# Performance work log

Hardware: AMD Instinct MI355X
Metric: run time of the kernel (lower is better)

## Reference

```python
import jax, jax.numpy as jnp
import numpy as np

T, D_IN, D_OUT, R, A = 8192, 4096, 4096, 16, 8  # tokens, in/out features, lora rank, n_adapters/segments


def setup_inputs() -> dict:
    key = jax.random.key(0)
    ks = jax.random.split(key, 8)
    x = jax.random.normal(ks[0], (T, D_IN), jnp.float32)
    base_w = jax.random.normal(ks[1], (D_OUT, D_IN), jnp.float32) * (D_IN ** -0.5)
    base_b = jax.random.normal(ks[2], (D_OUT,), jnp.float32)
    wa = jax.random.normal(ks[3], (A, D_IN, R), jnp.float32) * (D_IN ** -0.5)
    wb = jax.random.normal(ks[4], (A, R, D_OUT), jnp.float32) * (R ** -0.5)
    scaling = jax.random.uniform(ks[5], (A,), jnp.float32, 0.5, 2.0)
    inner = jnp.sort(jax.random.randint(ks[6], (A - 1,), 0, T)).astype(jnp.int32)
    segment = jnp.concatenate([jnp.zeros(1, jnp.int32), inner, jnp.full((1,), T, jnp.int32)])  # [A+1] boundaries
    lora_ids = jax.random.randint(ks[7], (A,), 0, A).astype(jnp.int32)  # adapter id per segment
    return {"x": x, "base_w": base_w, "base_b": base_b, "wa": wa, "wb": wb,
            "scaling": scaling, "segment": segment, "lora_ids": lora_ids}


def reference(x, base_w, base_b, wa, wb, scaling, segment, lora_ids):
    # base dense layer: result = base_layer(x)
    result = x @ base_w.T + base_b  # [T, D_OUT]
    # per-token segment id (segments are contiguous token ranges), then adapter id
    token_pos = jnp.arange(x.shape[0])
    token_seg = jnp.clip(jnp.searchsorted(segment, token_pos, side='right') - 1, 0, segment.shape[0] - 2)
    token_lora = lora_ids[token_seg]  # [T] adapter id per token
    # grouped rank-r GEMM (SGMV-style add_lora): h_t = x_t @ wa[id_t]; lora_t = h_t @ wb[id_t]
    onehot = jax.nn.one_hot(token_lora, wa.shape[0], dtype=x.dtype)  # [T, A]
    h = jnp.einsum('td,adr->tar', x, wa) * onehot[:, :, None]  # [T, A, R], masked to own adapter
    lora = jnp.einsum('tar,aro->to', h, wb)  # [T, D_OUT]
    # per-token scaling = repeat_interleave(scaling[lora_ids], lora_len)
    lora = lora * scaling[token_lora][:, None]
    return result + lora
```

## Files before the change

### kernel.cpp

```cpp
#include <hip/hip_runtime.h>

#define T_TOK 8192
#define DIN   4096
#define DOUTF 4096
#define RANK  16

#define BM 256
#define BN 256
#define BK 128
#define NT (DIN / BK)
#define NPAIR (NT / 2)

typedef __attribute__((ext_vector_type(4))) float f32x4;
typedef __attribute__((ext_vector_type(4))) int   i32x4;
typedef __attribute__((ext_vector_type(8))) short bf16x8;

#define GLB_PTR(p) ((const __attribute__((address_space(1))) void*)(p))
#define LDS_PTR(p) ((__attribute__((address_space(3))) void*)(p))

__device__ __forceinline__ unsigned short f2bf(float f) {
  unsigned u = __float_as_uint(f);
  u = (u + 0x7fffu + ((u >> 16) & 1u)) >> 16;
  return (unsigned short)u;
}

__global__ __launch_bounds__(256) void prep(const float* __restrict__ x,
                                            const float* __restrict__ base_w,
                                            const float* __restrict__ wa,
                                            const float* __restrict__ scaling,
                                            const int* __restrict__ segment,
                                            const int* __restrict__ lora_ids,
                                            signed char* __restrict__ xq,
                                            float* __restrict__ sx,
                                            signed char* __restrict__ wq,
                                            float* __restrict__ sw,
                                            float* __restrict__ hbuf,
                                            unsigned short* __restrict__ hb16,
                                            int* __restrict__ tokid) {
  const int lane = threadIdx.x & 63;
  const int wave = threadIdx.x >> 6;

  if (blockIdx.x >= 512) {
    const int row = (blockIdx.x - 512) * 4 + wave;
    const float* rp = base_w + (size_t)row * DIN;
    f32x4 v[16];
    float amax = 0.f;
#pragma unroll
    for (int it = 0; it < 16; ++it) {
      v[it] = *(const f32x4*)(rp + it * 256 + lane * 4);
#pragma unroll
      for (int e = 0; e < 4; ++e) amax = fmaxf(amax, fabsf(v[it][e]));
    }
#pragma unroll
    for (int o = 1; o < 64; o <<= 1) amax = fmaxf(amax, __shfl_xor(amax, o));
    const float inv = amax > 0.f ? 127.0f / amax : 0.f;
    if (lane == 0) sw[row] = amax * (1.0f / 127.0f);
    signed char* op = wq + (size_t)row * DIN;
#pragma unroll
    for (int it = 0; it < 16; ++it) {
      const int q0 = (int)rintf(v[it][0] * inv);
      const int q1 = (int)rintf(v[it][1] * inv);
      const int q2 = (int)rintf(v[it][2] * inv);
      const int q3 = (int)rintf(v[it][3] * inv);
      *(int*)(op + it * 256 + lane * 4) =
          (q0 & 255) | ((q1 & 255) << 8) | ((q2 & 255) << 16) | ((q3 & 255) << 24);
    }
    return;
  }

  const int t0 = blockIdx.x * 16 + wave * 4;

  int ids[4]; float sc[4];
#pragma unroll
  for (int q = 0; q < 4; ++q) {
    int t = t0 + q;
    int s = 0;
#pragma unroll
    for (int i = 1; i < 8; ++i)
      if (t >= segment[i]) s = i;
    int id = lora_ids[s];
    ids[q] = id;
    sc[q] = scaling[id];
  }

  float acc[4][16];
  float amax[4] = {0.f, 0.f, 0.f, 0.f};
#pragma unroll
  for (int q = 0; q < 4; ++q)
#pragma unroll
    for (int r = 0; r < 16; ++r) acc[q][r] = 0.f;

  const bool same = (ids[0] == ids[1]) && (ids[1] == ids[2]) && (ids[2] == ids[3]);
  const int dbase = lane * 4;

  if (same) {
    const float* wrow = wa + (size_t)ids[0] * DIN * RANK;
#pragma unroll 2
    for (int it = 0; it < 16; ++it) {
      const int d = it * 256 + dbase;
      f32x4 xv[4];
#pragma unroll
      for (int q = 0; q < 4; ++q) {
        xv[q] = *(const f32x4*)(x + (size_t)(t0 + q) * DIN + d);
#pragma unroll
        for (int e = 0; e < 4; ++e) amax[q] = fmaxf(amax[q], fabsf(xv[q][e]));
      }
#pragma unroll
      for (int dd = 0; dd < 4; ++dd) {
        const f32x4* wp = (const f32x4*)(wrow + (size_t)(d + dd) * RANK);
        f32x4 w0 = wp[0], w1 = wp[1], w2 = wp[2], w3 = wp[3];
#pragma unroll
        for (int q = 0; q < 4; ++q) {
          const float xs = xv[q][dd];
#pragma unroll
          for (int r = 0; r < 4; ++r) {
            acc[q][r]      += xs * w0[r];
            acc[q][r + 4]  += xs * w1[r];
            acc[q][r + 8]  += xs * w2[r];
            acc[q][r + 12] += xs * w3[r];
          }
        }
      }
    }
  } else {
#pragma unroll
    for (int q = 0; q < 4; ++q) {
      const float* wrow = wa + (size_t)ids[q] * DIN * RANK;
      for (int it = 0; it < 16; ++it) {
        const int d = it * 256 + dbase;
        f32x4 xv = *(const f32x4*)(x + (size_t)(t0 + q) * DIN + d);
#pragma unroll
        for (int e = 0; e < 4; ++e) amax[q] = fmaxf(amax[q], fabsf(xv[e]));
#pragma unroll
        for (int dd = 0; dd < 4; ++dd) {
          const f32x4* wp = (const f32x4*)(wrow + (size_t)(d + dd) * RANK);
          f32x4 w0 = wp[0], w1 = wp[1], w2 = wp[2], w3 = wp[3];
          const float xs = xv[dd];
#pragma unroll
          for (int r = 0; r < 4; ++r) {
            acc[q][r]      += xs * w0[r];
            acc[q][r + 4]  += xs * w1[r];
            acc[q][r + 8]  += xs * w2[r];
            acc[q][r + 12] += xs * w3[r];
          }
        }
      }
    }
  }

#pragma unroll
  for (int q = 0; q < 4; ++q) {
#pragma unroll
    for (int r = 0; r < 16; ++r) {
      float v = acc[q][r];
      v += __shfl_xor(v, 1);
      v += __shfl_xor(v, 2);
      v += __shfl_xor(v, 4);
      v += __shfl_xor(v, 8);
      v += __shfl_xor(v, 16);
      v += __shfl_xor(v, 32);
      acc[q][r] = v;
    }
    if (lane == 0) {
      int t = t0 + q;
      tokid[t] = ids[q];
#pragma unroll
      for (int r = 0; r < 16; ++r) {
        float v = sc[q] * acc[q][r];
        hbuf[t * RANK + r] = v;
        hb16[t * RANK + r] = f2bf(v);
      }
    }
  }

#pragma unroll
  for (int q = 0; q < 4; ++q) {
    float am = amax[q];
#pragma unroll
    for (int o = 1; o < 64; o <<= 1) am = fmaxf(am, __shfl_xor(am, o));
    const float inv = am > 0.f ? 127.0f / am : 0.f;
    if (lane == 0) sx[t0 + q] = am * (1.0f / 127.0f);
    const float* rp = x + (size_t)(t0 + q) * DIN;
    signed char* op = xq + (size_t)(t0 + q) * DIN;
#pragma unroll 4
    for (int it = 0; it < 16; ++it) {
      f32x4 v = *(const f32x4*)(rp + it * 256 + dbase);
      const int q0 = (int)rintf(v[0] * inv);
      const int q1 = (int)rintf(v[1] * inv);
      const int q2 = (int)rintf(v[2] * inv);
      const int q3 = (int)rintf(v[3] * inv);
      *(int*)(op + it * 256 + dbase) =
          (q0 & 255) | ((q1 & 255) << 8) | ((q2 & 255) << 16) | ((q3 & 255) << 24);
    }
  }
}

__global__ __launch_bounds__(512, 2) void gemm_fused(const signed char* __restrict__ A_,
                                                     const signed char* __restrict__ B_,
                                                     const float* __restrict__ bias,
                                                     const float* __restrict__ hbuf,
                                                     const unsigned short* __restrict__ hb16,
                                                     const int* __restrict__ tokid,
                                                     const float* __restrict__ wbt,
                                                     const float* __restrict__ sxv,
                                                     const float* __restrict__ swv,
                                                     float* __restrict__ out) {
  __shared__ __align__(16) signed char As[2][BM * BK];
  __shared__ __align__(16) signed char Bs[2][BN * BK];
  __shared__ int s_nb;

  const int tid = threadIdx.x;
  const int lane = tid & 63;
  const int wave = tid >> 6;
  const int wr = wave >> 2;
  const int wn = wave & 3;

  const int bsw = (blockIdx.x & 7) * 64 + (blockIdx.x >> 3);
  const int brow = (bsw >> 4) * BM;
  const int bcol = (bsw & 15) * BN;

  i32x4 acc[8][4] = {};

  const int g = lane >> 4;
  const int rsel = lane & 15;
  const int low3 = rsel & 7;

#define STAGE1(dst, bufp, h, tt, src, rb0)                                             \
  {                                                                                    \
    _Pragma("unroll")                                                                  \
    for (int i = 0; i < 2; ++i) {                                                      \
      const int lin2 = i * 512 + tid;                                                  \
      const int rr = lin2 >> 3;                                                        \
      const int klog = ((lin2 & 7) ^ (rr & 7)) * 16;                        \
      const signed char* gp = (src) + (size_t)((rb0) + (h) * 128 + rr) * DIN + (tt) * BK + klog; \
      __builtin_amdgcn_global_load_lds(GLB_PTR(gp), LDS_PTR(&dst[bufp][(h) * 16384 + lin2 * 16]), 16, 0, 0); \
    }                                                                                  \
  }

#define RD_B(p)                                                                        \
  _Pragma("unroll") for (int kk = 0; kk < 2; ++kk)                                     \
  _Pragma("unroll") for (int n = 0; n < 4; ++n)                                        \
    bfr[n][kk] = *(const i32x4*)(&Bs[p][(wn * 64 + n * 16 + rsel) * BK + (((kk) * 4 + g) ^ low3) * 16]);

#define RD_A(AF, p, mo, kk)                                                            \
  _Pragma("unroll") for (int mi = 0; mi < 4; ++mi)                                     \
    AF[mi] = *(const i32x4*)(&As[p][(wr * 128 + ((mo) + mi) * 16 + rsel) * BK + (((kk) * 4 + g) ^ low3) * 16]);

#define MFMA16(mo, kk, AF)                                                             \
  _Pragma("unroll") for (int mi = 0; mi < 4; ++mi)                                     \
  _Pragma("unroll") for (int n = 0; n < 4; ++n)                                        \
    acc[(mo) + mi][n] = __builtin_amdgcn_mfma_i32_16x16x64_i8(AF[mi], bfr[n][kk],      \
                                                              acc[(mo) + mi][n], 0, 0, 0)

#define PH_OPEN()                                                                      \
  asm volatile("" ::: "memory");                                                       \
  __builtin_amdgcn_s_barrier();                                                        \
  asm volatile("s_waitcnt lgkmcnt(0)" ::: "memory");                                   \
  __builtin_amdgcn_sched_barrier(0);                                                   \
  __builtin_amdgcn_s_setprio(1)

#define PH_CLOSE()                                                                     \
  __builtin_amdgcn_s_setprio(0);                                                       \
  asm volatile("" ::: "memory");                                                       \
  __builtin_amdgcn_s_barrier();                                                        \
  asm volatile("" ::: "memory")

#define PH_CLOSE_VM(N)                                                                 \
  __builtin_amdgcn_s_setprio(0);                                                       \
  asm volatile("s_waitcnt vmcnt(" #N ")" ::: "memory");                                \
  __builtin_amdgcn_s_barrier();                                                        \
  asm volatile("" ::: "memory")

  STAGE1(As, 0, 0, 0, A_, brow);
  STAGE1(As, 0, 1, 0, A_, brow);
  STAGE1(Bs, 0, 0, 0, B_, bcol);
  STAGE1(Bs, 0, 1, 0, B_, bcol);
  STAGE1(Bs, 1, 0, 1, B_, bcol);
  STAGE1(Bs, 1, 1, 1, B_, bcol);
  asm volatile("s_waitcnt vmcnt(4)" ::: "memory");
  __builtin_amdgcn_s_barrier();
  asm volatile("" ::: "memory");

  for (int j = 0; j < NPAIR - 1; ++j) {
    const int v = 2 * j + 1;
    i32x4 bfr[4][2], afA[4], afB[4];
    RD_B(0); RD_A(afA, 0, 0, 0);
    STAGE1(As, 1, 0, v, A_, brow);
    PH_OPEN(); MFMA16(0, 0, afA); PH_CLOSE();
    RD_A(afB, 0, 4, 0);
    STAGE1(As, 1, 1, v, A_, brow);
    PH_OPEN(); MFMA16(4, 0, afB); PH_CLOSE();
    RD_A(afA, 0, 0, 1);
    STAGE1(Bs, 0, 0, v + 1, B_, bcol);
    PH_OPEN(); MFMA16(0, 1, afA); PH_CLOSE();
    RD_A(afB, 0, 4, 1);
    STAGE1(Bs, 0, 1, v + 1, B_, bcol);
    PH_OPEN(); MFMA16(4, 1, afB); PH_CLOSE_VM(4);
    RD_B(1); RD_A(afA, 1, 0, 0);
    STAGE1(As, 0, 0, v + 1, A_, brow);
    PH_OPEN(); MFMA16(0, 0, afA); PH_CLOSE();
    RD_A(afB, 1, 4, 0);
    STAGE1(As, 0, 1, v + 1, A_, brow);
    PH_OPEN(); MFMA16(4, 0, afB); PH_CLOSE();
    RD_A(afA, 1, 0, 1);
    STAGE1(Bs, 1, 0, v + 2, B_, bcol);
    PH_OPEN(); MFMA16(0, 1, afA); PH_CLOSE();
    RD_A(afB, 1, 4, 1);
    STAGE1(Bs, 1, 1, v + 2, B_, bcol);
    PH_OPEN(); MFMA16(4, 1, afB); PH_CLOSE_VM(4);
  }

  {
    const int v = NT - 1;
    i32x4 bfr[4][2], afA[4], afB[4];
    RD_B(0); RD_A(afA, 0, 0, 0);
    STAGE1(As, 1, 0, v, A_, brow);
    PH_OPEN(); MFMA16(0, 0, afA); PH_CLOSE();
    RD_A(afB, 0, 4, 0);
    STAGE1(As, 1, 1, v, A_, brow);
    PH_OPEN(); MFMA16(4, 0, afB); PH_CLOSE();
    RD_A(afA, 0, 0, 1);
    PH_OPEN(); MFMA16(0, 1, afA); PH_CLOSE();
    RD_A(afB, 0, 4, 1);
    PH_OPEN(); MFMA16(4, 1, afB); PH_CLOSE_VM(0);
    RD_B(1); RD_A(afA, 1, 0, 0);
    PH_OPEN(); MFMA16(0, 0, afA); PH_CLOSE();
    RD_A(afB, 1, 4, 0);
    PH_OPEN(); MFMA16(4, 0, afB); PH_CLOSE();
    RD_A(afA, 1, 0, 1);
    PH_OPEN(); MFMA16(0, 1, afA); PH_CLOSE();
    RD_A(afB, 1, 4, 1);
    PH_OPEN(); MFMA16(4, 1, afB); PH_CLOSE();
  }

  const int rb = brow + wr * 128;
  const int cb = bcol + wn * 64;
  const int crow = g * 4;
  const int ccol = rsel;

  if (tid == 0) s_nb = 0;
  __syncthreads();
  if (tid >= 1 && tid < BM) {
    if (tokid[brow + tid] != tokid[brow + tid - 1]) atomicAdd(&s_nb, 1);
  }
  __syncthreads();
  const int nb = s_nb;
  const int idLo = tokid[brow];
  const int idHi = tokid[brow + BM - 1];

  float biasn[4], swn[4];
#pragma unroll
  for (int n = 0; n < 4; ++n) {
    biasn[n] = bias[cb + n * 16 + ccol];
    swn[n] = swv[cb + n * 16 + ccol];
  }

  f32x4 facc[8][4];
#pragma unroll
  for (int m = 0; m < 8; ++m) {
    float sxr[4];
#pragma unroll
    for (int jj = 0; jj < 4; ++jj) sxr[jj] = sxv[rb + m * 16 + crow + jj];
#pragma unroll
    for (int n = 0; n < 4; ++n)
#pragma unroll
      for (int jj = 0; jj < 4; ++jj)
        facc[m][n][jj] = (float)acc[m][n][jj] * (sxr[jj] * swn[n]);
  }

  if (nb <= 1) {
    const int myId = (g < 2) ? idLo : idHi;
    const int maskId = (g < 2) ? idLo : ((nb == 0) ? 0x80000000 : idHi);
    const float* wbase = wbt + (size_t)myId * RANK * DOUTF + (size_t)((g & 1) * 8) * DOUTF;
    bf16x8 bext[4];
#pragma unroll
    for (int n = 0; n < 4; ++n) {
      const int col = cb + n * 16 + ccol;
#pragma unroll
      for (int jj = 0; jj < 8; ++jj)
        bext[n][jj] = (short)f2bf(wbase[(size_t)jj * DOUTF + col]);
    }
#pragma unroll
    for (int m = 0; m < 8; ++m) {
      const int row = rb + m * 16 + rsel;
      const int rid = tokid[row];
      bf16x8 av = {};
      if (rid == maskId)
        av = *(const bf16x8*)(hb16 + (size_t)row * RANK + (g & 1) * 8);
#pragma unroll
      for (int n = 0; n < 4; ++n)
        facc[m][n] = __builtin_amdgcn_mfma_f32_16x16x32_bf16(av, bext[n], facc[m][n], 0, 0, 0);
    }
#pragma unroll
    for (int m = 0; m < 8; ++m) {
#pragma unroll
      for (int jj = 0; jj < 4; ++jj) {
        const int row = rb + m * 16 + crow + jj;
        float* orow = out + (size_t)row * DOUTF;
#pragma unroll
        for (int n = 0; n < 4; ++n)
          orow[cb + n * 16 + ccol] = facc[m][n][jj] + biasn[n];
      }
    }
  } else {
#pragma unroll
    for (int m = 0; m < 8; ++m) {
#pragma unroll
      for (int jj = 0; jj < 4; ++jj) {
        const int row = rb + m * 16 + crow + jj;
        const float4* hp = (const float4*)(hbuf + (size_t)row * RANK);
        float4 h0 = hp[0], h1 = hp[1], h2 = hp[2], h3 = hp[3];
        float hv[16] = {h0.x, h0.y, h0.z, h0.w, h1.x, h1.y, h1.z, h1.w,
                        h2.x, h2.y, h2.z, h2.w, h3.x, h3.y, h3.z, h3.w};
        const float* wrow = wbt + (size_t)tokid[row] * RANK * DOUTF;
        float* orow = out + (size_t)row * DOUTF;
#pragma unroll
        for (int n = 0; n < 4; ++n) {
          const int col = cb + n * 16 + ccol;
          float vsum = facc[m][n][jj] + biasn[n];
#pragma unroll
          for (int r = 0; r < 16; ++r) vsum += hv[r] * wrow[(size_t)r * DOUTF + col];
          orow[col] = vsum;
        }
      }
    }
  }
#undef STAGE1
#undef RD_A
#undef RD_B
#undef MFMA16
#undef PH_OPEN
#undef PH_CLOSE
#undef PH_CLOSE_VM
}

extern "C" void kernel_launch(void* const* d_in, const int* in_sizes, int n_in,
                              void* d_out, int out_size, void* d_ws, size_t ws_size,
                              hipStream_t stream) {
  const float* x       = (const float*)d_in[0];
  const float* base_w  = (const float*)d_in[1];
  const float* base_b  = (const float*)d_in[2];
  const float* wa      = (const float*)d_in[3];
  const float* wb      = (const float*)d_in[4];
  const float* scaling = (const float*)d_in[5];
  const int*   segment = (const int*)d_in[6];
  const int*   lora_id = (const int*)d_in[7];
  float* out = (float*)d_out;

  char* ws = (char*)d_ws;
  signed char* xq = (signed char*)ws;
  signed char* wq = (signed char*)(ws + (size_t)T_TOK * DIN);
  float* sx   = (float*)(ws + (size_t)T_TOK * DIN + (size_t)DOUTF * DIN);
  float* sw   = sx + T_TOK;
  float* hbuf = sw + DOUTF;
  int* tokid  = (int*)(hbuf + (size_t)T_TOK * RANK);
  unsigned short* hb16 = (unsigned short*)(tokid + T_TOK);

  prep<<<512 + DOUTF / 4, 256, 0, stream>>>(x, base_w, wa, scaling, segment, lora_id,
                                            xq, sx, wq, sw, hbuf, hb16, tokid);
  gemm_fused<<<(T_TOK / BM) * (DOUTF / BN), 512, 0, stream>>>(xq, wq, base_b, hbuf,
                                                              hb16, tokid, wb, sx, sw,
                                                              out);
}
```

Baseline: 299.0 us.

## Compute LoRA-A projection in prep with bf16 MFMA over 64-token blocks

The prep kernel's token path now handles 64 tokens per block instead of 16. Each block builds the list of adapters present in its tokens, stages each adapter's wa chunk in LDS as bf16, and computes the rank-16 projection with 16x16x32 bf16 MFMA instructions instead of scalar FMAs with cross-lane shuffle reductions. The int8 quantisation of x is rewritten so each thread writes 16 bytes per row. This reduces the ALU and shuffle work in the h computation, but it lowers h precision to bf16 inputs, re-reads x for every adapter present in the block, and adds block-level syncs.

Result: slower. 328.8 us (+10.0%).

```diff
diff --git a/kernel.cpp b/kernel.cpp
--- a/kernel.cpp
+++ b/kernel.cpp
@@ -37,11 +37,12 @@
                                             float* __restrict__ hbuf,
                                             unsigned short* __restrict__ hb16,
                                             int* __restrict__ tokid) {
-  const int lane = threadIdx.x & 63;
-  const int wave = threadIdx.x >> 6;
-
-  if (blockIdx.x >= 512) {
-    const int row = (blockIdx.x - 512) * 4 + wave;
+  const int tid = threadIdx.x;
+  const int lane = tid & 63;
+  const int wave = tid >> 6;
+
+  if (blockIdx.x >= 128) {
+    const int row = (blockIdx.x - 128) * 4 + wave;
     const float* rp = base_w + (size_t)row * DIN;
     f32x4 v[16];
     float amax = 0.f;
@@ -68,130 +69,124 @@
     return;
   }
 
-  const int t0 = blockIdx.x * 16 + wave * 4;
-
-  int ids[4]; float sc[4];
-#pragma unroll
-  for (int q = 0; q < 4; ++q) {
-    int t = t0 + q;
+  __shared__ __align__(16) unsigned short wch[16][520];
+  __shared__ float amax_l[64];
+  __shared__ int ids_l[64];
+  __shared__ int alist[8];
+  __shared__ int s_na;
+
+  const int T0 = blockIdx.x * 64;
+  const int Tw = T0 + wave * 16;
+  const int r15 = lane & 15;
+  const int kg = lane >> 4;
+
+  if (tid < 64) {
+    const int t = T0 + tid;
     int s = 0;
 #pragma unroll
     for (int i = 1; i < 8; ++i)
       if (t >= segment[i]) s = i;
-    int id = lora_ids[s];
-    ids[q] = id;
-    sc[q] = scaling[id];
-  }
-
-  float acc[4][16];
-  float amax[4] = {0.f, 0.f, 0.f, 0.f};
-#pragma unroll
-  for (int q = 0; q < 4; ++q)
-#pragma unroll
-    for (int r = 0; r < 16; ++r) acc[q][r] = 0.f;
-
-  const bool same = (ids[0] == ids[1]) && (ids[1] == ids[2]) && (ids[2] == ids[3]);
-  const int dbase = lane * 4;
-
-  if (same) {
-    const float* wrow = wa + (size_t)ids[0] * DIN * RANK;
-#pragma unroll 2
-    for (int it = 0; it < 16; ++it) {
-      const int d = it * 256 + dbase;
-      f32x4 xv[4];
-#pragma unroll
-      for (int q = 0; q < 4; ++q) {
-        xv[q] = *(const f32x4*)(x + (size_t)(t0 + q) * DIN + d);
-#pragma unroll
-        for (int e = 0; e < 4; ++e) amax[q] = fmaxf(amax[q], fabsf(xv[q][e]));
-      }
-#pragma unroll
-      for (int dd = 0; dd < 4; ++dd) {
-        const f32x4* wp = (const f32x4*)(wrow + (size_t)(d + dd) * RANK);
-        f32x4 w0 = wp[0], w1 = wp[1], w2 = wp[2], w3 = wp[3];
-#pragma unroll
-        for (int q = 0; q < 4; ++q) {
-          const float xs = xv[q][dd];
-#pragma unroll
-          for (int r = 0; r < 4; ++r) {
-            acc[q][r]      += xs * w0[r];
-            acc[q][r + 4]  += xs * w1[r];
-            acc[q][r + 8]  += xs * w2[r];
-            acc[q][r + 12] += xs * w3[r];
-          }
+    ids_l[tid] = lora_ids[s];
+  }
+  __syncthreads();
+  if (tid == 0) {
+    int na = 0;
+    for (int i = 0; i < 64; ++i) {
+      const int id = ids_l[i];
+      bool dup = false;
+      for (int q = 0; q < na; ++q) dup = dup || (alist[q] == id);
+      if (!dup) alist[na++] = id;
+    }
+    s_na = na;
+  }
+  __syncthreads();
+
+  const int myId = ids_l[wave * 16 + r15];
+  const int myTok = Tw + r15;
+  const int na = s_na;
+
+  f32x4 hacc = {0.f, 0.f, 0.f, 0.f};
+  float amax = 0.f;
+
+  for (int ai = 0; ai < na; ++ai) {
+    const int a = alist[ai];
+    const float* wabase = wa + (size_t)a * (DIN * RANK);
+    const unsigned long long mm = __ballot(myId == a);
+    const bool active = (mm != 0ull);
+    for (int c = 0; c < 8; ++c) {
+      __syncthreads();
+      {
+        const float* gp = wabase + (size_t)(c * 512 + 2 * tid) * RANK;
+        f32x4 w[8];
+#pragma unroll
+        for (int i = 0; i < 8; ++i) w[i] = *(const f32x4*)(gp + i * 4);
+#pragma unroll
+        for (int r = 0; r < 16; ++r) {
+          const unsigned lo = f2bf(w[r >> 2][r & 3]);
+          const unsigned hi = f2bf(w[4 + (r >> 2)][r & 3]);
+          *(unsigned*)&wch[r][2 * tid] = lo | (hi << 16);
         }
       }
-    }
-  } else {
-#pragma unroll
-    for (int q = 0; q < 4; ++q) {
-      const float* wrow = wa + (size_t)ids[q] * DIN * RANK;
-      for (int it = 0; it < 16; ++it) {
-        const int d = it * 256 + dbase;
-        f32x4 xv = *(const f32x4*)(x + (size_t)(t0 + q) * DIN + d);
-#pragma unroll
-        for (int e = 0; e < 4; ++e) amax[q] = fmaxf(amax[q], fabsf(xv[e]));
-#pragma unroll
-        for (int dd = 0; dd < 4; ++dd) {
-          const f32x4* wp = (const f32x4*)(wrow + (size_t)(d + dd) * RANK);
-          f32x4 w0 = wp[0], w1 = wp[1], w2 = wp[2], w3 = wp[3];
-          const float xs = xv[dd];
-#pragma unroll
-          for (int r = 0; r < 4; ++r) {
-            acc[q][r]      += xs * w0[r];
-            acc[q][r + 4]  += xs * w1[r];
-            acc[q][r + 8]  += xs * w2[r];
-            acc[q][r + 12] += xs * w3[r];
+      __syncthreads();
+      if (ai == 0 || active) {
+#pragma unroll 4
+        for (int s = 0; s < 16; ++s) {
+          const int kl = s * 32 + kg * 8;
+          const float* xp = x + (size_t)myTok * DIN + c * 512 + kl;
+          f32x4 x0 = *(const f32x4*)xp;
+          f32x4 x1 = *(const f32x4*)(xp + 4);
+          if (ai == 0) {
+#pragma unroll
+            for (int e = 0; e < 4; ++e)
+              amax = fmaxf(amax, fmaxf(fabsf(x0[e]), fabsf(x1[e])));
           }
+          bf16x8 af;
+#pragma unroll
+          for (int e = 0; e < 4; ++e) {
+            af[e] = (short)f2bf(x0[e]);
+            af[4 + e] = (short)f2bf(x1[e]);
+          }
+          if (myId != a) af = (bf16x8){0, 0, 0, 0, 0, 0, 0, 0};
+          const bf16x8 bf = *(const bf16x8*)&wch[r15][kl];
+          hacc = __builtin_amdgcn_mfma_f32_16x16x32_bf16(af, bf, hacc, 0, 0, 0);
         }
       }
     }
   }
 
-#pragma unroll
-  for (int q = 0; q < 4; ++q) {
-#pragma unroll
-    for (int r = 0; r < 16; ++r) {
-      float v = acc[q][r];
-      v += __shfl_xor(v, 1);
-      v += __shfl_xor(v, 2);
-      v += __shfl_xor(v, 4);
-      v += __shfl_xor(v, 8);
-      v += __shfl_xor(v, 16);
-      v += __shfl_xor(v, 32);
-      acc[q][r] = v;
-    }
-    if (lane == 0) {
-      int t = t0 + q;
-      tokid[t] = ids[q];
-#pragma unroll
-      for (int r = 0; r < 16; ++r) {
-        float v = sc[q] * acc[q][r];
-        hbuf[t * RANK + r] = v;
-        hb16[t * RANK + r] = f2bf(v);
-      }
-    }
-  }
-
-#pragma unroll
-  for (int q = 0; q < 4; ++q) {
-    float am = amax[q];
-#pragma unroll
-    for (int o = 1; o < 64; o <<= 1) am = fmaxf(am, __shfl_xor(am, o));
+  amax = fmaxf(amax, __shfl_xor(amax, 16));
+  amax = fmaxf(amax, __shfl_xor(amax, 32));
+  if (lane < 16) amax_l[wave * 16 + lane] = amax;
+
+#pragma unroll
+  for (int e = 0; e < 4; ++e) {
+    const int li = wave * 16 + kg * 4 + e;
+    const int t = T0 + li;
+    const float sc = scaling[ids_l[li]];
+    const float hv = hacc[e] * sc;
+    hbuf[t * RANK + r15] = hv;
+    hb16[t * RANK + r15] = f2bf(hv);
+  }
+
+  __syncthreads();
+  if (tid < 64) {
+    sx[T0 + tid] = amax_l[tid] * (1.0f / 127.0f);
+    tokid[T0 + tid] = ids_l[tid];
+  }
+
+  for (int row = 0; row < 64; ++row) {
+    const float am = amax_l[row];
     const float inv = am > 0.f ? 127.0f / am : 0.f;
-    if (lane == 0) sx[t0 + q] = am * (1.0f / 127.0f);
-    const float* rp = x + (size_t)(t0 + q) * DIN;
-    signed char* op = xq + (size_t)(t0 + q) * DIN;
-#pragma unroll 4
-    for (int it = 0; it < 16; ++it) {
-      f32x4 v = *(const f32x4*)(rp + it * 256 + dbase);
-      const int q0 = (int)rintf(v[0] * inv);
-      const int q1 = (int)rintf(v[1] * inv);
-      const int q2 = (int)rintf(v[2] * inv);
-      const int q3 = (int)rintf(v[3] * inv);
-      *(int*)(op + it * 256 + dbase) =
-          (q0 & 255) | ((q1 & 255) << 8) | ((q2 & 255) << 16) | ((q3 & 255) << 24);
-    }
+    const float* rp = x + (size_t)(T0 + row) * DIN + tid * 16;
+    signed char* op = xq + (size_t)(T0 + row) * DIN + tid * 16;
+    i32x4 pk;
+#pragma unroll
+    for (int i = 0; i < 4; ++i) {
+      f32x4 v = *(const f32x4*)(rp + i * 4);
+      pk[i] = ((int)rintf(v[0] * inv) & 255) | (((int)rintf(v[1] * inv) & 255) << 8) |
+              (((int)rintf(v[2] * inv) & 255) << 16) | (((int)rintf(v[3] * inv) & 255) << 24);
+    }
+    *(i32x4*)op = pk;
   }
 }
 
@@ -456,7 +451,7 @@
   int* tokid  = (int*)(hbuf + (size_t)T_TOK * RANK);
   unsigned short* hb16 = (unsigned short*)(tokid + T_TOK);
 
-  prep<<<512 + DOUTF / 4, 256, 0, stream>>>(x, base_w, wa, scaling, segment, lora_id,
+  prep<<<128 + DOUTF / 4, 256, 0, stream>>>(x, base_w, wa, scaling, segment, lora_id,
                                             xq, sx, wq, sw, hbuf, hb16, tokid);
   gemm_fused<<<(T_TOK / BM) * (DOUTF / BN), 512, 0, stream>>>(xq, wq, base_b, hbuf,
                                                               hb16, tokid, wb, sx, sw,
```

## Shrink GEMM tile to 128x128 with a simple double-buffered loop

Applied to the files above, without the earlier changes.

Replaces the 256x256-tile, 512-thread int8 GEMM and its hand-phased barrier/setprio pipeline with a 128x128 tile run by 256 threads. The K loop becomes a plain double-buffered loop that prefetches two K-steps ahead. This raises block count and occupancy at the cost of less data reuse per tile, twice the global/LDS traffic per output, and a less finely interleaved schedule. The block swizzle and epilogue are adjusted to the new tile.

New measurement: 291.1 us. 2.6% less time.

```diff
diff --git a/kernel.cpp b/kernel.cpp
--- a/kernel.cpp
+++ b/kernel.cpp
@@ -5,11 +5,10 @@
 #define DOUTF 4096
 #define RANK  16
 
-#define BM 256
-#define BN 256
-#define BK 128
-#define NT (DIN / BK)
-#define NPAIR (NT / 2)
+#define GBM 128
+#define GBN 128
+#define BK  128
+#define NT  (DIN / BK)
 
 typedef __attribute__((ext_vector_type(4))) float f32x4;
 typedef __attribute__((ext_vector_type(4))) int   i32x4;
@@ -195,7 +194,7 @@
   }
 }
 
-__global__ __launch_bounds__(512, 2) void gemm_fused(const signed char* __restrict__ A_,
+__global__ __launch_bounds__(256, 2) void gemm_fused(const signed char* __restrict__ A_,
                                                      const signed char* __restrict__ B_,
                                                      const float* __restrict__ bias,
                                                      const float* __restrict__ hbuf,
@@ -205,148 +204,100 @@
                                                      const float* __restrict__ sxv,
                                                      const float* __restrict__ swv,
                                                      float* __restrict__ out) {
-  __shared__ __align__(16) signed char As[2][BM * BK];
-  __shared__ __align__(16) signed char Bs[2][BN * BK];
+  __shared__ __align__(16) signed char As[2][GBM * BK];
+  __shared__ __align__(16) signed char Bs[2][GBN * BK];
   __shared__ int s_nb;
 
   const int tid = threadIdx.x;
   const int lane = tid & 63;
   const int wave = tid >> 6;
-  const int wr = wave >> 2;
-  const int wn = wave & 3;
-
-  const int bsw = (blockIdx.x & 7) * 64 + (blockIdx.x >> 3);
-  const int brow = (bsw >> 4) * BM;
-  const int bcol = (bsw & 15) * BN;
-
-  i32x4 acc[8][4] = {};
+  const int wr = wave >> 1;
+  const int wc = wave & 1;
+
+  const int bsw = (blockIdx.x & 7) * 256 + (blockIdx.x >> 3);
+  const int brow = (bsw >> 5) * GBM;
+  const int bcol = (bsw & 31) * GBN;
+
+  i32x4 acc[4][4] = {};
 
   const int g = lane >> 4;
   const int rsel = lane & 15;
   const int low3 = rsel & 7;
 
-#define STAGE1(dst, bufp, h, tt, src, rb0)                                             \
+#define STAGE(p, tt)                                                                   \
   {                                                                                    \
     _Pragma("unroll")                                                                  \
-    for (int i = 0; i < 2; ++i) {                                                      \
-      const int lin2 = i * 512 + tid;                                                  \
-      const int rr = lin2 >> 3;                                                        \
-      const int klog = ((lin2 & 7) ^ (rr & 7)) * 16;                        \
-      const signed char* gp = (src) + (size_t)((rb0) + (h) * 128 + rr) * DIN + (tt) * BK + klog; \
-      __builtin_amdgcn_global_load_lds(GLB_PTR(gp), LDS_PTR(&dst[bufp][(h) * 16384 + lin2 * 16]), 16, 0, 0); \
+    for (int i = 0; i < 4; ++i) {                                                      \
+      const int lin = i * 256 + tid;                                      \
+      const int rr = lin >> 3;                                         \
+      const int klog = ((lin & 7) ^ (rr & 7)) * 16;                         \
+      const signed char* gA = A_ + (size_t)(brow + rr) * DIN + (tt) * BK + klog;       \
+      const signed char* gB = B_ + (size_t)(bcol + rr) * DIN + (tt) * BK + klog;       \
+      __builtin_amdgcn_global_load_lds(GLB_PTR(gA), LDS_PTR(&As[p][lin * 16]), 16, 0, 0); \
+      __builtin_amdgcn_global_load_lds(GLB_PTR(gB), LDS_PTR(&Bs[p][lin * 16]), 16, 0, 0); \
     }                                                                                  \
   }
 
-#define RD_B(p)                                                                        \
-  _Pragma("unroll") for (int kk = 0; kk < 2; ++kk)                                     \
-  _Pragma("unroll") for (int n = 0; n < 4; ++n)                                        \
-    bfr[n][kk] = *(const i32x4*)(&Bs[p][(wn * 64 + n * 16 + rsel) * BK + (((kk) * 4 + g) ^ low3) * 16]);
-
-#define RD_A(AF, p, mo, kk)                                                            \
-  _Pragma("unroll") for (int mi = 0; mi < 4; ++mi)                                     \
-    AF[mi] = *(const i32x4*)(&As[p][(wr * 128 + ((mo) + mi) * 16 + rsel) * BK + (((kk) * 4 + g) ^ low3) * 16]);
-
-#define MFMA16(mo, kk, AF)                                                             \
-  _Pragma("unroll") for (int mi = 0; mi < 4; ++mi)                                     \
-  _Pragma("unroll") for (int n = 0; n < 4; ++n)                                        \
-    acc[(mo) + mi][n] = __builtin_amdgcn_mfma_i32_16x16x64_i8(AF[mi], bfr[n][kk],      \
-                                                              acc[(mo) + mi][n], 0, 0, 0)
-
-#define PH_OPEN()                                                                      \
-  asm volatile("" ::: "memory");                                                       \
-  __builtin_amdgcn_s_barrier();                                                        \
-  asm volatile("s_waitcnt lgkmcnt(0)" ::: "memory");                                   \
-  __builtin_amdgcn_sched_barrier(0);                                                   \
-  __builtin_amdgcn_s_setprio(1)
-
-#define PH_CLOSE()                                                                     \
-  __builtin_amdgcn_s_setprio(0);                                                       \
-  asm volatile("" ::: "memory");                                                       \
-  __builtin_amdgcn_s_barrier();                                                        \
-  asm volatile("" ::: "memory")
-
-#define PH_CLOSE_VM(N)                                                                 \
-  __builtin_amdgcn_s_setprio(0);                                                       \
-  asm volatile("s_waitcnt vmcnt(" #N ")" ::: "memory");                                \
-  __builtin_amdgcn_s_barrier();                                                        \
-  asm volatile("" ::: "memory")
-
-  STAGE1(As, 0, 0, 0, A_, brow);
-  STAGE1(As, 0, 1, 0, A_, brow);
-  STAGE1(Bs, 0, 0, 0, B_, bcol);
-  STAGE1(Bs, 0, 1, 0, B_, bcol);
-  STAGE1(Bs, 1, 0, 1, B_, bcol);
-  STAGE1(Bs, 1, 1, 1, B_, bcol);
-  asm volatile("s_waitcnt vmcnt(4)" ::: "memory");
+  STAGE(0, 0);
+  STAGE(1, 1);
+  asm volatile("s_waitcnt vmcnt(8)" ::: "memory");
   __builtin_amdgcn_s_barrier();
   asm volatile("" ::: "memory");
 
-  for (int j = 0; j < NPAIR - 1; ++j) {
-    const int v = 2 * j + 1;
-    i32x4 bfr[4][2], afA[4], afB[4];
-    RD_B(0); RD_A(afA, 0, 0, 0);
-    STAGE1(As, 1, 0, v, A_, brow);
-    PH_OPEN(); MFMA16(0, 0, afA); PH_CLOSE();
-    RD_A(afB, 0, 4, 0);
-    STAGE1(As, 1, 1, v, A_, brow);
-    PH_OPEN(); MFMA16(4, 0, afB); PH_CLOSE();
-    RD_A(afA, 0, 0, 1);
-    STAGE1(Bs, 0, 0, v + 1, B_, bcol);
-    PH_OPEN(); MFMA16(0, 1, afA); PH_CLOSE();
-    RD_A(afB, 0, 4, 1);
-    STAGE1(Bs, 0, 1, v + 1, B_, bcol);
-    PH_OPEN(); MFMA16(4, 1, afB); PH_CLOSE_VM(4);
-    RD_B(1); RD_A(afA, 1, 0, 0);
-    STAGE1(As, 0, 0, v + 1, A_, brow);
-    PH_OPEN(); MFMA16(0, 0, afA); PH_CLOSE();
-    RD_A(afB, 1, 4, 0);
-    STAGE1(As, 0, 1, v + 1, A_, brow);
-    PH_OPEN(); MFMA16(4, 0, afB); PH_CLOSE();
-    RD_A(afA, 1, 0, 1);
-    STAGE1(Bs, 1, 0, v + 2, B_, bcol);
-    PH_OPEN(); MFMA16(0, 1, afA); PH_CLOSE();
-    RD_A(afB, 1, 4, 1);
-    STAGE1(Bs, 1, 1, v + 2, B_, bcol);
-    PH_OPEN(); MFMA16(4, 1, afB); PH_CLOSE_VM(4);
-  }
-
-  {
-    const int v = NT - 1;
-    i32x4 bfr[4][2], afA[4], afB[4];
-    RD_B(0); RD_A(afA, 0, 0, 0);
-    STAGE1(As, 1, 0, v, A_, brow);
-    PH_OPEN(); MFMA16(0, 0, afA); PH_CLOSE();
-    RD_A(afB, 0, 4, 0);
-    STAGE1(As, 1, 1, v, A_, brow);
-    PH_OPEN(); MFMA16(4, 0, afB); PH_CLOSE();
-    RD_A(afA, 0, 0, 1);
-    PH_OPEN(); MFMA16(0, 1, afA); PH_CLOSE();
-    RD_A(afB, 0, 4, 1);
-    PH_OPEN(); MFMA16(4, 1, afB); PH_CLOSE_VM(0);
-    RD_B(1); RD_A(afA, 1, 0, 0);
-    PH_OPEN(); MFMA16(0, 0, afA); PH_CLOSE();
-    RD_A(afB, 1, 4, 0);
-    PH_OPEN(); MFMA16(4, 0, afB); PH_CLOSE();
-    RD_A(afA, 1, 0, 1);
-    PH_OPEN(); MFMA16(0, 1, afA); PH_CLOSE();
-    RD_A(afB, 1, 4, 1);
-    PH_OPEN(); MFMA16(4, 1, afB); PH_CLOSE();
-  }
-
-  const int rb = brow + wr * 128;
-  const int cb = bcol + wn * 64;
+  for (int t = 0; t < NT; ++t) {
+    const int p = t & 1;
+
+    i32x4 bfr[2][4], afr[2][4];
+#pragma unroll
+    for (int kk = 0; kk < 2; ++kk) {
+      const int ph = ((kk * 4 + g) ^ low3) * 16;
+#pragma unroll
+      for (int n = 0; n < 4; ++n)
+        bfr[kk][n] = *(const i32x4*)(&Bs[p][(wc * 64 + n * 16 + rsel) * BK + ph]);
+#pragma unroll
+      for (int m = 0; m < 4; ++m)
+        afr[kk][m] = *(const i32x4*)(&As[p][(wr * 64 + m * 16 + rsel) * BK + ph]);
+    }
+
+    __builtin_amdgcn_s_setprio(1);
+#pragma unroll
+    for (int kk = 0; kk < 2; ++kk)
+#pragma unroll
+      for (int m = 0; m < 4; ++m)
+#pragma unroll
+        for (int n = 0; n < 4; ++n)
+          acc[m][n] = __builtin_amdgcn_mfma_i32_16x16x64_i8(afr[kk][m], bfr[kk][n],
+                                                            acc[m][n], 0, 0, 0);
+    __builtin_amdgcn_s_setprio(0);
+
+    asm volatile("" ::: "memory");
+    __builtin_amdgcn_s_barrier();
+    asm volatile("" ::: "memory");
+
+    if (t + 2 < NT) {
+      STAGE(p, t + 2);
+      asm volatile("s_waitcnt vmcnt(8)" ::: "memory");
+    } else if (t + 1 < NT) {
+      asm volatile("s_waitcnt vmcnt(0)" ::: "memory");
+    }
+    __builtin_amdgcn_s_barrier();
+    asm volatile("" ::: "memory");
+  }
+
+  const int rb = brow + wr * 64;
+  const int cb = bcol + wc * 64;
   const int crow = g * 4;
   const int ccol = rsel;
 
   if (tid == 0) s_nb = 0;
   __syncthreads();
-  if (tid >= 1 && tid < BM) {
+  if (tid >= 1 && tid < GBM) {
     if (tokid[brow + tid] != tokid[brow + tid - 1]) atomicAdd(&s_nb, 1);
   }
   __syncthreads();
   const int nb = s_nb;
   const int idLo = tokid[brow];
-  const int idHi = tokid[brow + BM - 1];
+  const int idHi = tokid[brow + GBM - 1];
 
   float biasn[4], swn[4];
 #pragma unroll
@@ -355,9 +306,9 @@
     swn[n] = swv[cb + n * 16 + ccol];
   }
 
-  f32x4 facc[8][4];
-#pragma unroll
-  for (int m = 0; m < 8; ++m) {
+  f32x4 facc[4][4];
+#pragma unroll
+  for (int m = 0; m < 4; ++m) {
     float sxr[4];
 #pragma unroll
     for (int jj = 0; jj < 4; ++jj) sxr[jj] = sxv[rb + m * 16 + crow + jj];
@@ -381,7 +332,7 @@
         bext[n][jj] = (short)f2bf(wbase[(size_t)jj * DOUTF + col]);
     }
 #pragma unroll
-    for (int m = 0; m < 8; ++m) {
+    for (int m = 0; m < 4; ++m) {
       const int row = rb + m * 16 + rsel;
       const int rid = tokid[row];
       bf16x8 av = {};
@@ -392,7 +343,7 @@
         facc[m][n] = __builtin_amdgcn_mfma_f32_16x16x32_bf16(av, bext[n], facc[m][n], 0, 0, 0);
     }
 #pragma unroll
-    for (int m = 0; m < 8; ++m) {
+    for (int m = 0; m < 4; ++m) {
 #pragma unroll
       for (int jj = 0; jj < 4; ++jj) {
         const int row = rb + m * 16 + crow + jj;
@@ -404,7 +355,7 @@
     }
   } else {
 #pragma unroll
-    for (int m = 0; m < 8; ++m) {
+    for (int m = 0; m < 4; ++m) {
 #pragma unroll
       for (int jj = 0; jj < 4; ++jj) {
         const int row = rb + m * 16 + crow + jj;
@@ -425,13 +376,7 @@
       }
     }
   }
-#undef STAGE1
-#undef RD_A
-#undef RD_B
-#undef MFMA16
-#undef PH_OPEN
-#undef PH_CLOSE
-#undef PH_CLOSE_VM
+#undef STAGE
 }
 
 extern "C" void kernel_launch(void* const* d_in, const int* in_sizes, int n_in,
@@ -458,7 +403,7 @@
 
   prep<<<512 + DOUTF / 4, 256, 0, stream>>>(x, base_w, wa, scaling, segment, lora_id,
                                             xq, sx, wq, sw, hbuf, hb16, tokid);
-  gemm_fused<<<(T_TOK / BM) * (DOUTF / BN), 512, 0, stream>>>(xq, wq, base_b, hbuf,
-                                                              hb16, tokid, wb, sx, sw,
-                                                              out);
+  gemm_fused<<<(T_TOK / GBM) * (DOUTF / GBN), 256, 0, stream>>>(xq, wq, base_b, hbuf,
+                                                                hb16, tokid, wb, sx, sw,
+                                                                out);
 }
```
